# Kernel tuning notes

Measured on AMD Instinct MI355X. Metric: run time of the kernel, lower is better.

## Reference

```python
import jax, jax.numpy as jnp
import numpy as np

N = 20000; E = 320000; G = 64; IN = 64; HID = 128; H = 8; HD = H * HID  # 1024


def setup_inputs() -> dict:
    key = jax.random.key(0)
    ks = jax.random.split(key, 32)
    inp = {}
    inp['x'] = jax.random.normal(ks[0], (N, IN), jnp.float32)
    inp['edge_index'] = jax.random.randint(ks[1], (2, E), 0, N, dtype=jnp.int64)
    inp['batch'] = jnp.sort(jax.random.randint(ks[2], (N,), 0, G, dtype=jnp.int64))
    dims_in = [IN, HD, HD]
    k = 3
    for i in range(3):
        d_in = dims_in[i]
        inp[f'gat_W{i}'] = jax.random.normal(ks[k], (d_in, HD), jnp.float32) * (1.0 / np.sqrt(d_in)); k += 1
        inp[f'gat_b{i}'] = jnp.zeros((HD,), jnp.float32)
        inp[f'att_src{i}'] = jax.random.normal(ks[k], (H, HID), jnp.float32) * 0.1; k += 1
        inp[f'att_dst{i}'] = jax.random.normal(ks[k], (H, HID), jnp.float32) * 0.1; k += 1
    for i in range(2):
        inp[f'boot_W{i}'] = jax.random.normal(ks[k], (HD, HD), jnp.float32) * (1.0 / np.sqrt(HD)); k += 1
        inp[f'boot_b{i}'] = jnp.zeros((HD,), jnp.float32)
    inp['clf_W1'] = jax.random.normal(ks[k], (HD, HID), jnp.float32) * (1.0 / np.sqrt(HD)); k += 1
    inp['clf_b1'] = jnp.zeros((HID,), jnp.float32)
    inp['clf_W2'] = jax.random.normal(ks[k], (HID, 2), jnp.float32) * (1.0 / np.sqrt(HID)); k += 1
    inp['clf_b2'] = jnp.zeros((2,), jnp.float32)
    return inp


def _gat_layer(x, W, b, a_src, a_dst, src, dst):
    # PyG GATConv (concat=True, self-loops already appended, eval mode => no dropout)
    h = (x @ W).reshape(N, H, HID)                      # [N,H,D]
    s = jnp.einsum('nhd,hd->nh', h, a_src)              # [N,H]
    t = jnp.einsum('nhd,hd->nh', h, a_dst)              # [N,H]
    e = jax.nn.leaky_relu(s[src] + t[dst], 0.2)         # [Etot,H]
    m = jax.ops.segment_max(e, dst, num_segments=N)     # segment softmax over incoming edges
    m = jnp.where(jnp.isfinite(m), m, 0.0)
    ex = jnp.exp(e - m[dst])
    denom = jax.ops.segment_sum(ex, dst, num_segments=N)
    alpha = ex / jnp.maximum(denom[dst], 1e-16)         # [Etot,H]
    out = jax.ops.segment_sum(alpha[:, :, None] * h[src], dst, num_segments=N)  # [N,H,D]
    return out.reshape(N, HD) + b


def reference(x, edge_index, batch,
              gat_W0, gat_b0, att_src0, att_dst0,
              gat_W1, gat_b1, att_src1, att_dst1,
              gat_W2, gat_b2, att_src2, att_dst2,
              boot_W0, boot_b0, boot_W1, boot_b1,
              clf_W1, clf_b1, clf_W2, clf_b2):
    loop = jnp.arange(N, dtype=edge_index.dtype)
    src = jnp.concatenate([edge_index[0], loop])
    dst = jnp.concatenate([edge_index[1], loop])
    gat = [(gat_W0, gat_b0, att_src0, att_dst0),
           (gat_W1, gat_b1, att_src1, att_dst1),
           (gat_W2, gat_b2, att_src2, att_dst2)]
    boot = [(boot_W0, boot_b0), (boot_W1, boot_b1)]
    h = x
    for i in range(3):
        W, b, a_s, a_d = gat[i]
        h = jax.nn.elu(_gat_layer(h, W, b, a_s, a_d, src, dst))
        if i < 2:
            noise = jax.random.normal(jax.random.key(100 + i), h.shape, h.dtype) * 0.1
            bW, bb = boot[i]
            h = (h + noise) @ bW + bb
    # global mean pool over graphs
    sums = jax.ops.segment_sum(h, batch, num_segments=G)        # [G,HD]
    cnts = jax.ops.segment_sum(jnp.ones((N,), h.dtype), batch, num_segments=G)
    g = sums / jnp.maximum(cnts, 1.0)[:, None]
    z = jax.nn.relu(g @ clf_W1 + clf_b1)                        # dropout = identity (eval)
    return z @ clf_W2 + clf_b2
```

## Files before the change

kernel.cpp:

```cpp
#include <hip/hip_runtime.h>
#include <stdint.h>

#define N_NODES 20000
#define N_EDGES 320000
#define E_TOT   (N_EDGES + N_NODES)
#define NGRAPH  64
#define DIN     64
#define DHID    128
#define NHEAD   8
#define HDIM    1024

typedef unsigned int u32;
typedef unsigned short u16;
typedef __bf16 bfx8 __attribute__((ext_vector_type(8)));
typedef float f32x4 __attribute__((ext_vector_type(4)));
typedef float f32x2 __attribute__((ext_vector_type(2)));

__device__ __forceinline__ u16 f2bf(float f){
  u32 u = __float_as_uint(f);
  u32 r = (u + 0x7FFFu + ((u >> 16) & 1u)) >> 16;
  return (u16)r;
}
__device__ __forceinline__ float bf2f(u16 v){
  return __uint_as_float(((u32)v) << 16);
}

typedef __attribute__((address_space(3))) u32 lds_u32_t;
typedef const __attribute__((address_space(1))) u32 glb_u32_t;
__device__ __forceinline__ void g2l16(const void* g, void* l){
  __builtin_amdgcn_global_load_lds((glb_u32_t*)(uintptr_t)g,
                                   (lds_u32_t*)(uintptr_t)l, 16, 0, 0);
}

__device__ __forceinline__ u32 rotl32(u32 x, int r){ return (x<<r) | (x>>(32-r)); }

__device__ __forceinline__ void threefry2x32(u32 k0, u32 k1, u32 x0, u32 x1,
                                             u32& y0, u32& y1){
  u32 k2 = k0 ^ k1 ^ 0x1BD11BDAu;
  x0 += k0; x1 += k1;
#define TFR(r) { x0 += x1; x1 = rotl32(x1, (r)); x1 ^= x0; }
  TFR(13) TFR(15) TFR(26) TFR(6)
  x0 += k1; x1 += k2 + 1u;
  TFR(17) TFR(29) TFR(16) TFR(24)
  x0 += k2; x1 += k0 + 2u;
  TFR(13) TFR(15) TFR(26) TFR(6)
  x0 += k0; x1 += k1 + 3u;
  TFR(17) TFR(29) TFR(16) TFR(24)
  x0 += k1; x1 += k2 + 4u;
  TFR(13) TFR(15) TFR(26) TFR(6)
  x0 += k2; x1 += k0 + 5u;
#undef TFR
  y0 = x0; y1 = x1;
}

__device__ __forceinline__ float erfinv_fast(float x){
  float t = fmaf(-x, x, 1.0f);
  float w = -__logf(t);
  float p;
  if (w < 5.0f){
    w -= 2.5f;
    p = 2.81022636e-08f;
    p = fmaf(p, w, 3.43273939e-07f);
    p = fmaf(p, w, -3.5233877e-06f);
    p = fmaf(p, w, -4.39150654e-06f);
    p = fmaf(p, w, 0.00021858087f);
    p = fmaf(p, w, -0.00125372503f);
    p = fmaf(p, w, -0.00417768164f);
    p = fmaf(p, w, 0.246640727f);
    p = fmaf(p, w, 1.50140941f);
  } else {
    w = sqrtf(w) - 3.0f;
    p = -0.000200214257f;
    p = fmaf(p, w, 0.000100950558f);
    p = fmaf(p, w, 0.00134934322f);
    p = fmaf(p, w, -0.00367342844f);
    p = fmaf(p, w, 0.00573950773f);
    p = fmaf(p, w, -0.0076224613f);
    p = fmaf(p, w, 0.00943887047f);
    p = fmaf(p, w, 1.00167406f);
    p = fmaf(p, w, 2.83297682f);
  }
  return p * x;
}

__device__ __forceinline__ float jax_normal(u32 seed, u32 i){
  u32 y0, y1;
  threefry2x32(0u, seed, 0u, i, y0, y1);
  u32 bits = y0 ^ y1;
  float f = __uint_as_float((bits >> 9) | 0x3f800000u) - 1.0f;
  float xx = fmaxf(-0.99999994f, fmaf(f, 2.0f, -0.99999994f));
  return 1.41421356f * erfinv_fast(xx);
}

__global__ __launch_bounds__(256) void prep_misc_kernel(const float* __restrict__ x,
    const float* __restrict__ W0, const float* __restrict__ W1,
    u16* __restrict__ xbf, u16* __restrict__ O0, u16* __restrict__ O1,
    const int* __restrict__ ei, const int* __restrict__ batch,
    int* __restrict__ cnt, int* __restrict__ gcnt){
  const int z = blockIdx.y;
  if (z < 3){
    const float* S = (z==0) ? W0 : (z==1) ? W1 : x;
    u16* D = (z==0) ? O0 : (z==1) ? O1 : xbf;
    const int total = (z==2) ? N_NODES*DIN : HDIM*HDIM;
    int i = (blockIdx.x*256 + threadIdx.x)*4;
    if (i < total){
      float4 v = *(const float4*)(S + i);
      D[i+0] = f2bf(v.x); D[i+1] = f2bf(v.y);
      D[i+2] = f2bf(v.z); D[i+3] = f2bf(v.w);
    }
  } else {
    int i = blockIdx.x*256 + threadIdx.x;
    if (i < N_EDGES) atomicAdd(&cnt[ei[N_EDGES + i]], 1);
    else if (i < E_TOT) atomicAdd(&gcnt[batch[i - N_EDGES]], 1);
  }
}

__global__ __launch_bounds__(256) void transpose_all_kernel(
    const float* __restrict__ W0, const float* __restrict__ W1,
    const float* __restrict__ W2,
    u16* __restrict__ T0, u16* __restrict__ T1, u16* __restrict__ T2){
  const int z = blockIdx.z;
  const float* W = (z==0)?W0:(z==1)?W1:W2;
  u16* T = (z==0)?T0:(z==1)?T1:T2;
  const int K = (z==0)?DIN:HDIM;
  const int bk = blockIdx.y*32;
  if (bk >= K) return;
  __shared__ float t[32][33];
  int bn = blockIdx.x*32;
  int lx = threadIdx.x & 31, ly = threadIdx.x >> 5;
#pragma unroll
  for (int r = 0; r < 32; r += 8)
    t[ly+r][lx] = W[(size_t)(bk+ly+r)*HDIM + bn + lx];
  __syncthreads();
#pragma unroll
  for (int r = 0; r < 32; r += 8)
    T[(size_t)(bn+ly+r)*K + bk + lx] = f2bf(t[lx][ly+r]);
}

__global__ __launch_bounds__(1024) void scan_pair_kernel(const int* __restrict__ cnt,
    int* __restrict__ rowptr, int* __restrict__ cursor, int* __restrict__ colidx,
    const int* __restrict__ gcnt, int* __restrict__ goff){
  if (blockIdx.x == 1){
    if (threadIdx.x == 0){
      int s = 0;
      for (int g = 0; g < NGRAPH; ++g){ goff[g] = s; s += gcnt[g]; }
      goff[NGRAPH] = s;
    }
    return;
  }
  __shared__ int wsum[16];
  __shared__ int carry_s;
  const int tid = threadIdx.x, lane = tid & 63, wv = tid >> 6;
  if (tid == 0){ carry_s = 0; rowptr[0] = 0; }
  __syncthreads();
  for (int base = 0; base < N_NODES; base += 1024){
    int i = base + tid;
    int v = (i < N_NODES) ? cnt[i] + 1 : 0;
    int s = v;
#pragma unroll
    for (int off = 1; off < 64; off <<= 1){
      int t = __shfl_up(s, off);
      if (lane >= off) s += t;
    }
    if (lane == 63) wsum[wv] = s;
    __syncthreads();
    if (wv == 0 && lane < 16){
      int ws = wsum[lane];
#pragma unroll
      for (int off = 1; off < 16; off <<= 1){
        int t = __shfl_up(ws, off);
        if (lane >= off) ws += t;
      }
      wsum[lane] = ws;
    }
    __syncthreads();
    int incl = s + ((wv > 0) ? wsum[wv-1] : 0) + carry_s;
    if (i < N_NODES){
      rowptr[i+1] = incl;
      const int slot = incl - v;
      colidx[slot] = i;
      cursor[i] = slot + 1;
    }
    __syncthreads();
    if (tid == 1023) carry_s = incl;
    __syncthreads();
  }
}

__global__ __launch_bounds__(256) void fill_edges_kernel(const int* __restrict__ ei,
    int* __restrict__ cursor, int* __restrict__ colidx){
  int e = blockIdx.x*256 + threadIdx.x;
  if (e < N_EDGES){
    int s = ei[e], d = ei[N_EDGES + e];
    int p = atomicAdd(&cursor[d], 1);
    colidx[p] = s;
  }
}

__device__ __forceinline__ void gemm_tile(const u16* __restrict__ A,
    const u16* __restrict__ BT, const float* __restrict__ bias,
    u16* __restrict__ Cb, int M, int K, int bm, int bn,
    u16* As, u16* Bs,
    const float* __restrict__ asrc, const float* __restrict__ adst,
    float* __restrict__ sbuf, float* __restrict__ tbuf){
  const int tid = threadIdx.x;
  const int lane = tid & 63, w = tid >> 6;
  const int wm = (w & 1)*64, wn = (w >> 1)*64;

  const int cid0 = tid, cid1 = 256 + tid;
  const int r0 = cid0 & 127, kc0 = cid0 >> 7;
  const int r1 = cid1 & 127, kc1 = cid1 >> 7;
  int ar0 = bm + r0; if (ar0 >= M) ar0 = M - 1;
  int ar1 = bm + r1; if (ar1 >= M) ar1 = M - 1;
  const u16* ag0 = A + (size_t)ar0*K + kc0*8;
  const u16* ag1 = A + (size_t)ar1*K + kc1*8;
  const u16* bg0 = BT + (size_t)(bn + r0)*K + kc0*8;
  const u16* bg1 = BT + (size_t)(bn + r1)*K + kc1*8;
  u16* al0 = As + cid0*8;  u16* al1 = As + cid1*8;
  u16* bl0 = Bs + cid0*8;  u16* bl1 = Bs + cid1*8;

  const int rowl = lane & 15, kg = lane >> 4;
  const bfx8* ap = (const bfx8*)(As + ((size_t)kg*128 + wm + rowl)*8);
  const bfx8* bp = (const bfx8*)(Bs + ((size_t)kg*128 + wn + rowl)*8);

  f32x4 acc[4][4] = {};
  for (int k0 = 0; k0 < K; k0 += 32){
    g2l16(ag0 + k0, al0);
    g2l16(ag1 + k0, al1);
    g2l16(bg0 + k0, bl0);
    g2l16(bg1 + k0, bl1);
    __syncthreads();
    bfx8 af[4], bfr[4];
#pragma unroll
    for (int i = 0; i < 4; ++i){ af[i] = ap[i*16]; bfr[i] = bp[i*16]; }
#pragma unroll
    for (int i = 0; i < 4; ++i)
#pragma unroll
      for (int j = 0; j < 4; ++j)
        acc[j][i] = __builtin_amdgcn_mfma_f32_16x16x32_bf16(bfr[j], af[i], acc[j][i], 0, 0, 0);
    __syncthreads();
  }

  const int quad = lane >> 4;
  const bool dost = (sbuf != nullptr);
  const int head = bn >> 7;
  float sl[4] = {0.f,0.f,0.f,0.f}, tl[4] = {0.f,0.f,0.f,0.f};
#pragma unroll
  for (int j = 0; j < 4; ++j){
    const int col0 = bn + wn + j*16 + quad*4;
    float4 bv = make_float4(0.f,0.f,0.f,0.f);
    if (bias) bv = *(const float4*)(bias + col0);
    float4 av = make_float4(0.f,0.f,0.f,0.f), dv = av;
    if (dost){
      const int d0 = col0 - bn;
      av = *(const float4*)(asrc + head*DHID + d0);
      dv = *(const float4*)(adst + head*DHID + d0);
    }
#pragma unroll
    for (int i = 0; i < 4; ++i){
      const int row = bm + wm + i*16 + rowl;
      const u16 p0 = f2bf(acc[j][i][0] + bv.x);
      const u16 p1 = f2bf(acc[j][i][1] + bv.y);
      const u16 p2 = f2bf(acc[j][i][2] + bv.z);
      const u16 p3 = f2bf(acc[j][i][3] + bv.w);
      if (row < M){
        uint2 pk;
        pk.x = (u32)p0 | ((u32)p1 << 16);
        pk.y = (u32)p2 | ((u32)p3 << 16);
        *(uint2*)(Cb + (size_t)row*HDIM + col0) = pk;
      }
      if (dost){
        const float c0 = bf2f(p0), c1 = bf2f(p1), c2 = bf2f(p2), c3 = bf2f(p3);
        sl[i] = fmaf(c0, av.x, fmaf(c1, av.y, fmaf(c2, av.z, fmaf(c3, av.w, sl[i]))));
        tl[i] = fmaf(c0, dv.x, fmaf(c1, dv.y, fmaf(c2, dv.z, fmaf(c3, dv.w, tl[i]))));
      }
    }
  }
  if (dost){
#pragma unroll
    for (int i = 0; i < 4; ++i){
      sl[i] += __shfl_xor(sl[i], 16); sl[i] += __shfl_xor(sl[i], 32);
      tl[i] += __shfl_xor(tl[i], 16); tl[i] += __shfl_xor(tl[i], 32);
    }
    float* sred = (float*)As;
    float* tred = sred + 128;
    if ((w >> 1) == 0 && quad == 0){
#pragma unroll
      for (int i = 0; i < 4; ++i){
        const int rl = wm + i*16 + rowl;
        sred[rl] = sl[i]; tred[rl] = tl[i];
      }
    }
    __syncthreads();
    if ((w >> 1) == 1 && quad == 0){
#pragma unroll
      for (int i = 0; i < 4; ++i){
        const int rl = wm + i*16 + rowl;
        const int row = bm + rl;
        if (row < M){
          sbuf[row*NHEAD + head] = sred[rl] + sl[i];
          tbuf[row*NHEAD + head] = tred[rl] + tl[i];
        }
      }
    }
  }
}

__global__ __launch_bounds__(256) void gemm_bf16(
    const u16* __restrict__ A, const u16* __restrict__ BT,
    const float* __restrict__ bias, u16* __restrict__ Cb, int M, int K,
    const float* __restrict__ asrc, const float* __restrict__ adst,
    float* __restrict__ sbuf, float* __restrict__ tbuf){
  __shared__ __align__(16) u16 As[4*128*8];
  __shared__ __align__(16) u16 Bs[4*128*8];
  const int kblk = blockIdx.y*8 + blockIdx.x;
  const int xc = kblk & 7, bq = (kblk >> 3) & 7, gq = kblk >> 6;
  const int bmi = gq*8 + xc;
  const int mt = (M + 127) >> 7;
  if (bmi >= mt) return;
  gemm_tile(A, BT, bias, Cb, M, K, bmi*128, bq*128, As, Bs,
            asrc, adst, sbuf, tbuf);
}

__global__ __launch_bounds__(256) void wf_bias_kernel(
    const u16* __restrict__ A0, const u16* __restrict__ B0, u16* __restrict__ C0,
    const u16* __restrict__ A1, const u16* __restrict__ B1, u16* __restrict__ C1,
    const float* __restrict__ bb0, const u16* __restrict__ gwt0,
    const float* __restrict__ bb1, const u16* __restrict__ gwt1,
    float* __restrict__ fb0, float* __restrict__ fb1){
  __shared__ __align__(16) u16 As[4*128*8];
  __shared__ __align__(16) u16 Bs[4*128*8];
  if (blockIdx.z < 2){
    const u16* A = blockIdx.z ? A1 : A0;
    const u16* B = blockIdx.z ? B1 : B0;
    u16* C = blockIdx.z ? C1 : C0;
    gemm_tile(A, B, nullptr, C, HDIM, HDIM, blockIdx.y*128, blockIdx.x*128,
              As, Bs, nullptr, nullptr, nullptr, nullptr);
  } else {
    const int kb = blockIdx.y*8 + blockIdx.x;
    const int wv = threadIdx.x >> 6, lane = threadIdx.x & 63;
    for (int idx = kb*4 + wv; idx < 2*HDIM; idx += 256){
      const int set = idx >> 10, n = idx & (HDIM-1);
      const float* bb = set ? bb1 : bb0;
      const u16* row = (set ? gwt1 : gwt0) + (size_t)n*HDIM + lane*16;
      const float* bp = bb + lane*16;
      float acc = 0.f;
#pragma unroll
      for (int k = 0; k < 16; ++k) acc = fmaf(bp[k], bf2f(row[k]), acc);
      for (int off = 32; off > 0; off >>= 1) acc += __shfl_down(acc, off);
      if (lane == 0) (set ? fb1 : fb0)[n] = acc;
    }
  }
}

__global__ __launch_bounds__(256) void gat_agg_kernel(const u16* __restrict__ hlin,
    const float* __restrict__ sbuf, const float* __restrict__ tbuf,
    const int* __restrict__ rowptr, const int* __restrict__ colidx,
    const float* __restrict__ bias, float* __restrict__ outf,
    u16* __restrict__ outbf, u32 seed){
  __shared__ float esh[64*NHEAD];
  __shared__ int   srcs[64];
  __shared__ float tn[NHEAD], mh[NHEAD], dsum[NHEAD], resc[NHEAD];
  const int n = blockIdx.x;
  const int tid = threadIdx.x;
  const int ht = tid >> 5;
  if (tid < NHEAD){
    tn[tid] = tbuf[n*NHEAD + tid];
    mh[tid] = -INFINITY;
    dsum[tid] = 0.0f;
  }
  const int row0 = rowptr[n];
  const int deg = rowptr[n+1] - row0;
  const char* hl = (const char*)hlin;
  const u32 tid8 = (u32)tid*8u;
  const char* sbase = (const char*)sbuf;
  f32x2 a01 = {0.f,0.f}, a23 = {0.f,0.f};
  f32x2 b01 = {0.f,0.f}, b23 = {0.f,0.f};
  for (int c = 0; c < deg; c += 64){
    const int nc = min(64, deg - c);
    __syncthreads();
    if (tid < nc) srcs[tid] = colidx[row0 + c + tid] << 11;
    __syncthreads();
    for (int it = tid; it < nc*NHEAD; it += 256){
      int j = it >> 3, hh = it & 7;
      const float* sp = (const float*)(sbase + (srcs[j] >> 6));
      float e = sp[hh] + tn[hh];
      esh[it] = (e > 0.f) ? e : 0.2f*e;
    }
    __syncthreads();
    if (tid < 64){
      const int hh = tid & 7, slot = tid >> 3;
      float mc = -INFINITY;
      for (int j = slot; j < nc; j += 8) mc = fmaxf(mc, esh[j*NHEAD+hh]);
      mc = fmaxf(mc, __shfl_xor(mc, 8));
      mc = fmaxf(mc, __shfl_xor(mc, 16));
      mc = fmaxf(mc, __shfl_xor(mc, 32));
      const float mold = mh[hh];
      const float mnew = fmaxf(mold, mc);
      float wsum = 0.f;
      for (int j = slot; j < nc; j += 8){
        float w = __expf(esh[j*NHEAD+hh] - mnew);
        esh[j*NHEAD+hh] = w;
        wsum += w;
      }
      wsum += __shfl_xor(wsum, 8);
      wsum += __shfl_xor(wsum, 16);
      wsum += __shfl_xor(wsum, 32);
      if (slot == 0){
        float r = (mold == -INFINITY) ? 0.0f : __expf(mold - mnew);
        dsum[hh] = fmaf(dsum[hh], r, wsum);
        mh[hh] = mnew;
        resc[hh] = r;
      }
    }
    __syncthreads();
    const float r = resc[ht];
    const f32x2 r2 = {r, r};
    a01 *= r2; a23 *= r2; b01 *= r2; b23 *= r2;
    int j = 0;
    for (; j + 2 <= nc; j += 2){
      const float w0 = esh[j*NHEAD + ht];
      const float w1 = esh[(j+1)*NHEAD + ht];
      const char* rp0 = hl + (u32)__builtin_amdgcn_readfirstlane(srcs[j]);
      const char* rp1 = hl + (u32)__builtin_amdgcn_readfirstlane(srcs[j+1]);
      const uint2 h0 = *(const uint2*)(rp0 + tid8);
      const uint2 h1 = *(const uint2*)(rp1 + tid8);
      const f32x2 w02 = {w0, w0}, w12 = {w1, w1};
      f32x2 v;
      v.x = __uint_as_float(h0.x << 16); v.y = __uint_as_float(h0.x & 0xffff0000u);
      a01 = __builtin_elementwise_fma(w02, v, a01);
      v.x = __uint_as_float(h0.y << 16); v.y = __uint_as_float(h0.y & 0xffff0000u);
      a23 = __builtin_elementwise_fma(w02, v, a23);
      v.x = __uint_as_float(h1.x << 16); v.y = __uint_as_float(h1.x & 0xffff0000u);
      b01 = __builtin_elementwise_fma(w12, v, b01);
      v.x = __uint_as_float(h1.y << 16); v.y = __uint_as_float(h1.y & 0xffff0000u);
      b23 = __builtin_elementwise_fma(w12, v, b23);
    }
    if (j < nc){
      const float w0 = esh[j*NHEAD + ht];
      const char* rp0 = hl + (u32)__builtin_amdgcn_readfirstlane(srcs[j]);
      const uint2 h0 = *(const uint2*)(rp0 + tid8);
      const f32x2 w02 = {w0, w0};
      f32x2 v;
      v.x = __uint_as_float(h0.x << 16); v.y = __uint_as_float(h0.x & 0xffff0000u);
      a01 = __builtin_elementwise_fma(w02, v, a01);
      v.x = __uint_as_float(h0.y << 16); v.y = __uint_as_float(h0.y & 0xffff0000u);
      a23 = __builtin_elementwise_fma(w02, v, a23);
    }
  }
  float4 acc = make_float4(a01.x + b01.x, a01.y + b01.y,
                           a23.x + b23.x, a23.y + b23.y);
  const float inv = 1.0f / fmaxf(dsum[ht], 1e-16f);
  const float4 bv = *(const float4*)(bias + tid*4);
  float4 o;
  o.x = fmaf(acc.x, inv, bv.x);
  o.y = fmaf(acc.y, inv, bv.y);
  o.z = fmaf(acc.z, inv, bv.z);
  o.w = fmaf(acc.w, inv, bv.w);
  o.x = (o.x > 0.f) ? o.x : __expf(o.x) - 1.0f;
  o.y = (o.y > 0.f) ? o.y : __expf(o.y) - 1.0f;
  o.z = (o.z > 0.f) ? o.z : __expf(o.z) - 1.0f;
  o.w = (o.w > 0.f) ? o.w : __expf(o.w) - 1.0f;
  if (outbf){
    const u32 ib = (u32)(n*HDIM + tid*4);
    ushort4 ov;
    ov.x = f2bf(fmaf(0.1f, jax_normal(seed, ib+0u), o.x));
    ov.y = f2bf(fmaf(0.1f, jax_normal(seed, ib+1u), o.y));
    ov.z = f2bf(fmaf(0.1f, jax_normal(seed, ib+2u), o.z));
    ov.w = f2bf(fmaf(0.1f, jax_normal(seed, ib+3u), o.w));
    *(ushort4*)(outbf + (size_t)n*HDIM + tid*4) = ov;
  } else {
    *(float4*)(outf + (size_t)n*HDIM + tid*4) = o;
  }
}

__global__ __launch_bounds__(256) void pool_clf_kernel(const float* __restrict__ h,
    const int* __restrict__ goff, const int* __restrict__ gcnt,
    const float* __restrict__ W1, const float* __restrict__ b1,
    const float* __restrict__ W2, const float* __restrict__ b2,
    float* __restrict__ out){
  __shared__ float gs[HDIM];
  __shared__ float z[DHID];
  const int g = blockIdx.x, tid = threadIdx.x;
  const int cb = tid*4;
  float4 acc = make_float4(0.f,0.f,0.f,0.f);
  const int n0 = goff[g], n1 = goff[g+1];
  for (int n = n0; n < n1; ++n){
    const float4 v = *(const float4*)(h + (size_t)n*HDIM + cb);
    acc.x += v.x; acc.y += v.y; acc.z += v.z; acc.w += v.w;
  }
  const float invc = 1.0f / fmaxf((float)gcnt[g], 1.0f);
  gs[cb+0] = acc.x*invc; gs[cb+1] = acc.y*invc;
  gs[cb+2] = acc.z*invc; gs[cb+3] = acc.w*invc;
  __syncthreads();
  if (tid < DHID){
    float a = b1[tid];
    for (int k = 0; k < HDIM; ++k) a = fmaf(gs[k], W1[k*DHID + tid], a);
    z[tid] = fmaxf(a, 0.0f);
  }
  __syncthreads();
  if (tid < 2){
    float o = b2[tid];
    for (int k = 0; k < DHID; ++k) o = fmaf(z[k], W2[k*2 + tid], o);
    out[g*2 + tid] = o;
  }
}

extern "C" void kernel_launch(void* const* d_in, const int* in_sizes, int n_in,
                              void* d_out, int out_size, void* d_ws, size_t ws_size,
                              hipStream_t stream){
  const float* x      = (const float*)d_in[0];
  const int*   ei     = (const int*)d_in[1];
  const int*   batch  = (const int*)d_in[2];
  const float* gatW[3]  = {(const float*)d_in[3],  (const float*)d_in[7],  (const float*)d_in[11]};
  const float* gatB[3]  = {(const float*)d_in[4],  (const float*)d_in[8],  (const float*)d_in[12]};
  const float* asrc[3]  = {(const float*)d_in[5],  (const float*)d_in[9],  (const float*)d_in[13]};
  const float* adst[3]  = {(const float*)d_in[6],  (const float*)d_in[10], (const float*)d_in[14]};
  const float* bootW[2] = {(const float*)d_in[15], (const float*)d_in[17]};
  const float* bootB[2] = {(const float*)d_in[16], (const float*)d_in[18]};
  const float* clfW1 = (const float*)d_in[19];
  const float* clfb1 = (const float*)d_in[20];
  const float* clfW2 = (const float*)d_in[21];
  const float* clfb2 = (const float*)d_in[22];
  float* outp = (float*)d_out;

  float* fws  = (float*)d_ws;
  float* hB   = fws;
  float* sbuf = hB + (size_t)N_NODES*HDIM;
  float* tbuf = sbuf + (size_t)N_NODES*NHEAD;
  float* fbias0 = tbuf + (size_t)N_NODES*NHEAD;
  float* fbias1 = fbias0 + HDIM;
  u16* xbf    = (u16*)(fbias1 + HDIM);
  u16* hAbf   = xbf + (size_t)N_NODES*DIN;
  u16* hBbf   = hAbf + (size_t)N_NODES*HDIM;
  u16* wt[3];
  wt[0] = hBbf + (size_t)N_NODES*HDIM;
  wt[1] = wt[0] + (size_t)HDIM*DIN;
  wt[2] = wt[1] + (size_t)HDIM*HDIM;
  u16* wnt0   = wt[2] + (size_t)HDIM*HDIM;
  u16* wnt1   = wnt0 + (size_t)HDIM*HDIM;
  u16* wf0    = wnt1 + (size_t)HDIM*HDIM;
  u16* wf1    = wf0 + (size_t)HDIM*HDIM;
  int* rowptr = (int*)(wf1 + (size_t)HDIM*HDIM);
  int* cursor = rowptr + (N_NODES+1);
  int* colidx = cursor + N_NODES;
  int* gcnt   = colidx + E_TOT;
  int* cnt    = gcnt + NGRAPH;
  int* goff   = cnt + N_NODES;

  hipMemsetAsync(gcnt, 0, (NGRAPH + N_NODES)*sizeof(int), stream);

  const int nb_e = (N_EDGES + 255)/256;

  prep_misc_kernel<<<dim3((E_TOT + 255)/256, 4), 256, 0, stream>>>(
      x, bootW[0], bootW[1], xbf, wnt0, wnt1, ei, batch, cnt, gcnt);
  transpose_all_kernel<<<dim3(HDIM/32, HDIM/32, 3), 256, 0, stream>>>(
      gatW[0], gatW[1], gatW[2], wt[0], wt[1], wt[2]);
  scan_pair_kernel<<<2, 1024, 0, stream>>>(cnt, rowptr, cursor, colidx, gcnt, goff);
  fill_edges_kernel<<<nb_e, 256, 0, stream>>>(ei, cursor, colidx);

  wf_bias_kernel<<<dim3(8, 8, 3), 256, 0, stream>>>(
      wt[1], wnt0, wf0, wt[2], wnt1, wf1,
      bootB[0], wt[1], bootB[1], wt[2], fbias0, fbias1);

  const int mt = (N_NODES + 127)/128;
  dim3 gemmGrid(8, (mt + 7)/8*8);

  gemm_bf16<<<gemmGrid, 256, 0, stream>>>(xbf, wt[0], nullptr, hAbf, N_NODES, DIN,
                                          asrc[0], adst[0], sbuf, tbuf);
  gat_agg_kernel<<<N_NODES, 256, 0, stream>>>(hAbf, sbuf, tbuf, rowptr, colidx,
                                              gatB[0], nullptr, hBbf, 100u);
  gemm_bf16<<<gemmGrid, 256, 0, stream>>>(hBbf, wf0, fbias0, hAbf, N_NODES, HDIM,
                                          asrc[1], adst[1], sbuf, tbuf);
  gat_agg_kernel<<<N_NODES, 256, 0, stream>>>(hAbf, sbuf, tbuf, rowptr, colidx,
                                              gatB[1], nullptr, hBbf, 101u);
  gemm_bf16<<<gemmGrid, 256, 0, stream>>>(hBbf, wf1, fbias1, hAbf, N_NODES, HDIM,
                                          asrc[2], adst[2], sbuf, tbuf);
  gat_agg_kernel<<<N_NODES, 256, 0, stream>>>(hAbf, sbuf, tbuf, rowptr, colidx,
                                              gatB[2], hB, nullptr, 0u);

  pool_clf_kernel<<<NGRAPH, 256, 0, stream>>>(hB, goff, gcnt,
                                              clfW1, clfb1, clfW2, clfb2, outp);
}
```

Before: 934.2 us.

## Use one wavefront per node in GAT aggregation and parallelize mean pooling

The aggregation kernel now assigns one 64-lane wavefront per destination node (four nodes per block), not one block per node. It computes the online softmax over chunks of 8 edges with cross-lane shuffles in place of shared memory and block barriers, and each lane gathers 32 bytes of the source feature row. Pooling is split into a kernel with many blocks that sums rows per graph using atomics, followed by a small classifier kernel. This removes the __syncthreads overhead and the serial per-graph row loop. In exchange it adds float atomics, which make the summation order nondeterministic, and more registers per lane.

```diff
diff --git a/kernel.cpp b/kernel.cpp
--- a/kernel.cpp
+++ b/kernel.cpp
@@ -23,6 +23,12 @@
 }
 __device__ __forceinline__ float bf2f(u16 v){
   return __uint_as_float(((u32)v) << 16);
+}
+__device__ __forceinline__ f32x2 up2(u32 u){
+  f32x2 v;
+  v.x = __uint_as_float(u << 16);
+  v.y = __uint_as_float(u & 0xffff0000u);
+  return v;
 }
 
 typedef __attribute__((address_space(3))) u32 lds_u32_t;
@@ -358,124 +364,158 @@
     const int* __restrict__ rowptr, const int* __restrict__ colidx,
     const float* __restrict__ bias, float* __restrict__ outf,
     u16* __restrict__ outbf, u32 seed){
-  __shared__ float esh[64*NHEAD];
-  __shared__ int   srcs[64];
-  __shared__ float tn[NHEAD], mh[NHEAD], dsum[NHEAD], resc[NHEAD];
-  const int n = blockIdx.x;
-  const int tid = threadIdx.x;
-  const int ht = tid >> 5;
-  if (tid < NHEAD){
-    tn[tid] = tbuf[n*NHEAD + tid];
-    mh[tid] = -INFINITY;
-    dsum[tid] = 0.0f;
-  }
+  const int tid  = threadIdx.x;
+  const int lane = tid & 63;
+  const int n    = blockIdx.x*4 + (tid >> 6);
+  const int jsub = lane >> 3;
+  const int hh   = lane & 7;
+  const int hA   = lane >> 3;
   const int row0 = rowptr[n];
-  const int deg = rowptr[n+1] - row0;
+  const int deg  = rowptr[n+1] - row0;
+  const float tn = tbuf[n*NHEAD + hh];
   const char* hl = (const char*)hlin;
-  const u32 tid8 = (u32)tid*8u;
-  const char* sbase = (const char*)sbuf;
-  f32x2 a01 = {0.f,0.f}, a23 = {0.f,0.f};
-  f32x2 b01 = {0.f,0.f}, b23 = {0.f,0.f};
-  for (int c = 0; c < deg; c += 64){
-    const int nc = min(64, deg - c);
-    __syncthreads();
-    if (tid < nc) srcs[tid] = colidx[row0 + c + tid] << 11;
-    __syncthreads();
-    for (int it = tid; it < nc*NHEAD; it += 256){
-      int j = it >> 3, hh = it & 7;
-      const float* sp = (const float*)(sbase + (srcs[j] >> 6));
-      float e = sp[hh] + tn[hh];
-      esh[it] = (e > 0.f) ? e : 0.2f*e;
-    }
-    __syncthreads();
-    if (tid < 64){
-      const int hh = tid & 7, slot = tid >> 3;
-      float mc = -INFINITY;
-      for (int j = slot; j < nc; j += 8) mc = fmaxf(mc, esh[j*NHEAD+hh]);
-      mc = fmaxf(mc, __shfl_xor(mc, 8));
-      mc = fmaxf(mc, __shfl_xor(mc, 16));
-      mc = fmaxf(mc, __shfl_xor(mc, 32));
-      const float mold = mh[hh];
-      const float mnew = fmaxf(mold, mc);
-      float wsum = 0.f;
-      for (int j = slot; j < nc; j += 8){
-        float w = __expf(esh[j*NHEAD+hh] - mnew);
-        esh[j*NHEAD+hh] = w;
-        wsum += w;
-      }
-      wsum += __shfl_xor(wsum, 8);
-      wsum += __shfl_xor(wsum, 16);
-      wsum += __shfl_xor(wsum, 32);
-      if (slot == 0){
-        float r = (mold == -INFINITY) ? 0.0f : __expf(mold - mnew);
-        dsum[hh] = fmaf(dsum[hh], r, wsum);
-        mh[hh] = mnew;
-        resc[hh] = r;
-      }
-    }
-    __syncthreads();
-    const float r = resc[ht];
-    const f32x2 r2 = {r, r};
-    a01 *= r2; a23 *= r2; b01 *= r2; b23 *= r2;
+  const u32 lb   = (u32)lane << 5;
+
+  f32x2 acc[8] = {};
+  float m_run = -INFINITY, d_run = 0.f;
+
+  for (int c = 0; c < deg; c += 8){
+    const int ne = min(8, deg - c);
+    const int jj = (jsub < ne) ? jsub : (ne - 1);
+    const int srcv = colidx[row0 + c + jj];
+    float e = sbuf[srcv*NHEAD + hh] + tn;
+    e = (e > 0.f) ? e : 0.2f*e;
+    if (jsub >= ne) e = -INFINITY;
+    float mc = e;
+    mc = fmaxf(mc, __shfl_xor(mc, 8));
+    mc = fmaxf(mc, __shfl_xor(mc, 16));
+    mc = fmaxf(mc, __shfl_xor(mc, 32));
+    const float mnew = fmaxf(m_run, mc);
+    const float w = __expf(e - mnew);
+    float ws = w;
+    ws += __shfl_xor(ws, 8);
+    ws += __shfl_xor(ws, 16);
+    ws += __shfl_xor(ws, 32);
+    const float r = (m_run == -INFINITY) ? 0.0f : __expf(m_run - mnew);
+    d_run = fmaf(d_run, r, ws);
+    m_run = mnew;
+    const float rA = __shfl(r, hA);
+    const f32x2 r2 = {rA, rA};
+#pragma unroll
+    for (int q = 0; q < 8; ++q) acc[q] *= r2;
     int j = 0;
-    for (; j + 2 <= nc; j += 2){
-      const float w0 = esh[j*NHEAD + ht];
-      const float w1 = esh[(j+1)*NHEAD + ht];
-      const char* rp0 = hl + (u32)__builtin_amdgcn_readfirstlane(srcs[j]);
-      const char* rp1 = hl + (u32)__builtin_amdgcn_readfirstlane(srcs[j+1]);
-      const uint2 h0 = *(const uint2*)(rp0 + tid8);
-      const uint2 h1 = *(const uint2*)(rp1 + tid8);
+    for (; j + 2 <= ne; j += 2){
+      const int s0 = __builtin_amdgcn_readlane(srcv, j*8);
+      const int s1 = __builtin_amdgcn_readlane(srcv, j*8 + 8);
+      const float w0 = __shfl(w, j*8 + hA);
+      const float w1 = __shfl(w, j*8 + 8 + hA);
+      const char* rp0 = hl + (((size_t)(u32)s0) << 11);
+      const char* rp1 = hl + (((size_t)(u32)s1) << 11);
+      const uint4 a0 = *(const uint4*)(rp0 + lb);
+      const uint4 a1 = *(const uint4*)(rp0 + lb + 16);
+      const uint4 b0 = *(const uint4*)(rp1 + lb);
+      const uint4 b1 = *(const uint4*)(rp1 + lb + 16);
       const f32x2 w02 = {w0, w0}, w12 = {w1, w1};
-      f32x2 v;
-      v.x = __uint_as_float(h0.x << 16); v.y = __uint_as_float(h0.x & 0xffff0000u);
-      a01 = __builtin_elementwise_fma(w02, v, a01);
-      v.x = __uint_as_float(h0.y << 16); v.y = __uint_as_float(h0.y & 0xffff0000u);
-      a23 = __builtin_elementwise_fma(w02, v, a23);
-      v.x = __uint_as_float(h1.x << 16); v.y = __uint_as_float(h1.x & 0xffff0000u);
-      b01 = __builtin_elementwise_fma(w12, v, b01);
-      v.x = __uint_as_float(h1.y << 16); v.y = __uint_as_float(h1.y & 0xffff0000u);
-      b23 = __builtin_elementwise_fma(w12, v, b23);
-    }
-    if (j < nc){
-      const float w0 = esh[j*NHEAD + ht];
-      const char* rp0 = hl + (u32)__builtin_amdgcn_readfirstlane(srcs[j]);
-      const uint2 h0 = *(const uint2*)(rp0 + tid8);
+      acc[0] = __builtin_elementwise_fma(w02, up2(a0.x), acc[0]);
+      acc[1] = __builtin_elementwise_fma(w02, up2(a0.y), acc[1]);
+      acc[2] = __builtin_elementwise_fma(w02, up2(a0.z), acc[2]);
+      acc[3] = __builtin_elementwise_fma(w02, up2(a0.w), acc[3]);
+      acc[4] = __builtin_elementwise_fma(w02, up2(a1.x), acc[4]);
+      acc[5] = __builtin_elementwise_fma(w02, up2(a1.y), acc[5]);
+      acc[6] = __builtin_elementwise_fma(w02, up2(a1.z), acc[6]);
+      acc[7] = __builtin_elementwise_fma(w02, up2(a1.w), acc[7]);
+      acc[0] = __builtin_elementwise_fma(w12, up2(b0.x), acc[0]);
+      acc[1] = __builtin_elementwise_fma(w12, up2(b0.y), acc[1]);
+      acc[2] = __builtin_elementwise_fma(w12, up2(b0.z), acc[2]);
+      acc[3] = __builtin_elementwise_fma(w12, up2(b0.w), acc[3]);
+      acc[4] = __builtin_elementwise_fma(w12, up2(b1.x), acc[4]);
+      acc[5] = __builtin_elementwise_fma(w12, up2(b1.y), acc[5]);
+      acc[6] = __builtin_elementwise_fma(w12, up2(b1.z), acc[6]);
+      acc[7] = __builtin_elementwise_fma(w12, up2(b1.w), acc[7]);
+    }
+    if (j < ne){
+      const int s0 = __builtin_amdgcn_readlane(srcv, j*8);
+      const float w0 = __shfl(w, j*8 + hA);
+      const char* rp0 = hl + (((size_t)(u32)s0) << 11);
+      const uint4 a0 = *(const uint4*)(rp0 + lb);
+      const uint4 a1 = *(const uint4*)(rp0 + lb + 16);
       const f32x2 w02 = {w0, w0};
-      f32x2 v;
-      v.x = __uint_as_float(h0.x << 16); v.y = __uint_as_float(h0.x & 0xffff0000u);
-      a01 = __builtin_elementwise_fma(w02, v, a01);
-      v.x = __uint_as_float(h0.y << 16); v.y = __uint_as_float(h0.y & 0xffff0000u);
-      a23 = __builtin_elementwise_fma(w02, v, a23);
-    }
-  }
-  float4 acc = make_float4(a01.x + b01.x, a01.y + b01.y,
-                           a23.x + b23.x, a23.y + b23.y);
-  const float inv = 1.0f / fmaxf(dsum[ht], 1e-16f);
-  const float4 bv = *(const float4*)(bias + tid*4);
-  float4 o;
-  o.x = fmaf(acc.x, inv, bv.x);
-  o.y = fmaf(acc.y, inv, bv.y);
-  o.z = fmaf(acc.z, inv, bv.z);
-  o.w = fmaf(acc.w, inv, bv.w);
-  o.x = (o.x > 0.f) ? o.x : __expf(o.x) - 1.0f;
-  o.y = (o.y > 0.f) ? o.y : __expf(o.y) - 1.0f;
-  o.z = (o.z > 0.f) ? o.z : __expf(o.z) - 1.0f;
-  o.w = (o.w > 0.f) ? o.w : __expf(o.w) - 1.0f;
+      acc[0] = __builtin_elementwise_fma(w02, up2(a0.x), acc[0]);
+      acc[1] = __builtin_elementwise_fma(w02, up2(a0.y), acc[1]);
+      acc[2] = __builtin_elementwise_fma(w02, up2(a0.z), acc[2]);
+      acc[3] = __builtin_elementwise_fma(w02, up2(a0.w), acc[3]);
+      acc[4] = __builtin_elementwise_fma(w02, up2(a1.x), acc[4]);
+      acc[5] = __builtin_elementwise_fma(w02, up2(a1.y), acc[5]);
+      acc[6] = __builtin_elementwise_fma(w02, up2(a1.z), acc[6]);
+      acc[7] = __builtin_elementwise_fma(w02, up2(a1.w), acc[7]);
+    }
+  }
+
+  const float dA = __shfl(d_run, hA);
+  const float invA = 1.0f / fmaxf(dA, 1e-16f);
+  float o[16];
+#pragma unroll
+  for (int q = 0; q < 8; ++q){ o[2*q] = acc[q].x; o[2*q+1] = acc[q].y; }
+  const float4* bp = (const float4*)(bias + lane*16);
+#pragma unroll
+  for (int q = 0; q < 4; ++q){
+    const float4 bv = bp[q];
+    o[4*q+0] = fmaf(o[4*q+0], invA, bv.x);
+    o[4*q+1] = fmaf(o[4*q+1], invA, bv.y);
+    o[4*q+2] = fmaf(o[4*q+2], invA, bv.z);
+    o[4*q+3] = fmaf(o[4*q+3], invA, bv.w);
+  }
+#pragma unroll
+  for (int k = 0; k < 16; ++k)
+    o[k] = (o[k] > 0.f) ? o[k] : __expf(o[k]) - 1.0f;
   if (outbf){
-    const u32 ib = (u32)(n*HDIM + tid*4);
-    ushort4 ov;
-    ov.x = f2bf(fmaf(0.1f, jax_normal(seed, ib+0u), o.x));
-    ov.y = f2bf(fmaf(0.1f, jax_normal(seed, ib+1u), o.y));
-    ov.z = f2bf(fmaf(0.1f, jax_normal(seed, ib+2u), o.z));
-    ov.w = f2bf(fmaf(0.1f, jax_normal(seed, ib+3u), o.w));
-    *(ushort4*)(outbf + (size_t)n*HDIM + tid*4) = ov;
+    const u32 ib = (u32)n*HDIM + (u32)lane*16u;
+    u32 pk[8];
+#pragma unroll
+    for (int q = 0; q < 8; ++q){
+      const float v0 = fmaf(0.1f, jax_normal(seed, ib + 2u*q + 0u), o[2*q+0]);
+      const float v1 = fmaf(0.1f, jax_normal(seed, ib + 2u*q + 1u), o[2*q+1]);
+      pk[q] = (u32)f2bf(v0) | ((u32)f2bf(v1) << 16);
+    }
+    uint4* dst = (uint4*)(outbf + (size_t)n*HDIM + lane*16);
+    dst[0] = make_uint4(pk[0], pk[1], pk[2], pk[3]);
+    dst[1] = make_uint4(pk[4], pk[5], pk[6], pk[7]);
   } else {
-    *(float4*)(outf + (size_t)n*HDIM + tid*4) = o;
-  }
-}
-
-__global__ __launch_bounds__(256) void pool_clf_kernel(const float* __restrict__ h,
-    const int* __restrict__ goff, const int* __restrict__ gcnt,
+    float4* dst = (float4*)(outf + (size_t)n*HDIM + lane*16);
+#pragma unroll
+    for (int q = 0; q < 4; ++q)
+      dst[q] = make_float4(o[4*q], o[4*q+1], o[4*q+2], o[4*q+3]);
+  }
+}
+
+__global__ __launch_bounds__(256) void pool_sum_kernel(const float* __restrict__ h,
+    const int* __restrict__ batch, float* __restrict__ gsum){
+  const int n0 = blockIdx.x*128;
+  const int n1 = min(n0 + 128, N_NODES);
+  const int cb = threadIdx.x*4;
+  float4 acc = make_float4(0.f,0.f,0.f,0.f);
+  int curg = batch[n0];
+  for (int n = n0; n < n1; ++n){
+    const int g = batch[n];
+    if (g != curg){
+      atomicAdd(&gsum[curg*HDIM + cb+0], acc.x);
+      atomicAdd(&gsum[curg*HDIM + cb+1], acc.y);
+      atomicAdd(&gsum[curg*HDIM + cb+2], acc.z);
+      atomicAdd(&gsum[curg*HDIM + cb+3], acc.w);
+      acc = make_float4(0.f,0.f,0.f,0.f);
+      curg = g;
+    }
+    const float4 v = *(const float4*)(h + (size_t)n*HDIM + cb);
+    acc.x += v.x; acc.y += v.y; acc.z += v.z; acc.w += v.w;
+  }
+  atomicAdd(&gsum[curg*HDIM + cb+0], acc.x);
+  atomicAdd(&gsum[curg*HDIM + cb+1], acc.y);
+  atomicAdd(&gsum[curg*HDIM + cb+2], acc.z);
+  atomicAdd(&gsum[curg*HDIM + cb+3], acc.w);
+}
+
+__global__ __launch_bounds__(256) void pool_clf_kernel(const float* __restrict__ gsum,
+    const int* __restrict__ gcnt,
     const float* __restrict__ W1, const float* __restrict__ b1,
     const float* __restrict__ W2, const float* __restrict__ b2,
     float* __restrict__ out){
@@ -483,15 +523,10 @@
   __shared__ float z[DHID];
   const int g = blockIdx.x, tid = threadIdx.x;
   const int cb = tid*4;
-  float4 acc = make_float4(0.f,0.f,0.f,0.f);
-  const int n0 = goff[g], n1 = goff[g+1];
-  for (int n = n0; n < n1; ++n){
-    const float4 v = *(const float4*)(h + (size_t)n*HDIM + cb);
-    acc.x += v.x; acc.y += v.y; acc.z += v.z; acc.w += v.w;
-  }
   const float invc = 1.0f / fmaxf((float)gcnt[g], 1.0f);
-  gs[cb+0] = acc.x*invc; gs[cb+1] = acc.y*invc;
-  gs[cb+2] = acc.z*invc; gs[cb+3] = acc.w*invc;
+  const float4 s = *(const float4*)(gsum + (size_t)g*HDIM + cb);
+  gs[cb+0] = s.x*invc; gs[cb+1] = s.y*invc;
+  gs[cb+2] = s.z*invc; gs[cb+3] = s.w*invc;
   __syncthreads();
   if (tid < DHID){
     float a = b1[tid];
@@ -546,9 +581,10 @@
   int* colidx = cursor + N_NODES;
   int* gcnt   = colidx + E_TOT;
   int* cnt    = gcnt + NGRAPH;
-  int* goff   = cnt + N_NODES;
-
-  hipMemsetAsync(gcnt, 0, (NGRAPH + N_NODES)*sizeof(int), stream);
+  float* gsum = (float*)(cnt + N_NODES);
+  int* goff   = (int*)(gsum + (size_t)NGRAPH*HDIM);
+
+  (void)hipMemsetAsync(gcnt, 0, (NGRAPH + N_NODES + NGRAPH*HDIM)*sizeof(int), stream);
 
   const int nb_e = (N_EDGES + 255)/256;
 
@@ -568,17 +604,18 @@
 
   gemm_bf16<<<gemmGrid, 256, 0, stream>>>(xbf, wt[0], nullptr, hAbf, N_NODES, DIN,
                                           asrc[0], adst[0], sbuf, tbuf);
-  gat_agg_kernel<<<N_NODES, 256, 0, stream>>>(hAbf, sbuf, tbuf, rowptr, colidx,
-                                              gatB[0], nullptr, hBbf, 100u);
+  gat_agg_kernel<<<N_NODES/4, 256, 0, stream>>>(hAbf, sbuf, tbuf, rowptr, colidx,
+                                                gatB[0], nullptr, hBbf, 100u);
   gemm_bf16<<<gemmGrid, 256, 0, stream>>>(hBbf, wf0, fbias0, hAbf, N_NODES, HDIM,
                                           asrc[1], adst[1], sbuf, tbuf);
-  gat_agg_kernel<<<N_NODES, 256, 0, stream>>>(hAbf, sbuf, tbuf, rowptr, colidx,
-                                              gatB[1], nullptr, hBbf, 101u);
+  gat_agg_kernel<<<N_NODES/4, 256, 0, stream>>>(hAbf, sbuf, tbuf, rowptr, colidx,
+                                                gatB[1], nullptr, hBbf, 101u);
   gemm_bf16<<<gemmGrid, 256, 0, stream>>>(hBbf, wf1, fbias1, hAbf, N_NODES, HDIM,
                                           asrc[2], adst[2], sbuf, tbuf);
-  gat_agg_kernel<<<N_NODES, 256, 0, stream>>>(hAbf, sbuf, tbuf, rowptr, colidx,
-                                              gatB[2], hB, nullptr, 0u);
-
-  pool_clf_kernel<<<NGRAPH, 256, 0, stream>>>(hB, goff, gcnt,
+  gat_agg_kernel<<<N_NODES/4, 256, 0, stream>>>(hAbf, sbuf, tbuf, rowptr, colidx,
+                                                gatB[2], hB, nullptr, 0u);
+
+  pool_sum_kernel<<<(N_NODES + 127)/128, 256, 0, stream>>>(hB, batch, gsum);
+  pool_clf_kernel<<<NGRAPH, 256, 0, stream>>>(gsum, gcnt,
                                               clfW1, clfb1, clfW2, clfb2, outp);
 }
```

After: 873.0 us. 1.07x faster.
